# Optimization experiments

Measured on AMD Instinct MI355X. Metric: run time of the kernel, lower is better.

## Reference

```python
import jax, jax.numpy as jnp
import numpy as np

NEG_INF = -1000000000.0
B, N, D, H, L, DFF = 4, 1024, 512, 8, 6, 2048
DH = D // H
R2 = 10.0 ** 2  # locality_radius^2
EPS = 1e-5


def setup_inputs() -> dict:
    key = jax.random.key(0)
    ks = jax.random.split(key, 16)
    s = 0.02
    inp = {
        "tokens": jax.random.normal(ks[0], (B, N, D), jnp.float32),
        "xy": jax.random.uniform(ks[1], (B, N, 2), jnp.float32) * 100.0,
        "Wq": jax.random.normal(ks[2], (L, D, D), jnp.float32) * s,
        "Wk": jax.random.normal(ks[3], (L, D, D), jnp.float32) * s,
        "Wv": jax.random.normal(ks[4], (L, D, D), jnp.float32) * s,
        "Wo": jax.random.normal(ks[5], (L, D, D), jnp.float32) * s,
        "bo": jnp.zeros((L, D), jnp.float32),
        "W1": jax.random.normal(ks[6], (L, D, DFF), jnp.float32) * s,
        "b1": jnp.zeros((L, DFF), jnp.float32),
        "W2": jax.random.normal(ks[7], (L, DFF, D), jnp.float32) * s,
        "b2": jnp.zeros((L, D), jnp.float32),
        "g1": jnp.ones((L, D), jnp.float32),
        "be1": jnp.zeros((L, D), jnp.float32),
        "g2": jnp.ones((L, D), jnp.float32),
        "be2": jnp.zeros((L, D), jnp.float32),
        "gf": jnp.ones((D,), jnp.float32),
        "bf": jnp.zeros((D,), jnp.float32),
        "alive": jax.random.randint(ks[8], (B, N), 0, 2, dtype=jnp.int32),
        "species": jax.random.randint(ks[9], (B, N), 0, 3, dtype=jnp.int32),
        "n_agents": 512,
    }
    return inp


def _ln(x, g, b):
    m = jnp.mean(x, axis=-1, keepdims=True)
    v = jnp.mean((x - m) ** 2, axis=-1, keepdims=True)
    return (x - m) * jax.lax.rsqrt(v + EPS) * g + b


def _build_bias(alive, xy, species, dtype):
    # (B,1,N,N) additive bias, broadcast over heads (original repeats per head)
    af = alive.astype(dtype)
    bias = (1.0 - af)[:, None, None, :] * NEG_INF  # dead keys
    d2 = jnp.sum((xy[:, :, None, :] - xy[:, None, :, :]) ** 2, axis=-1)  # (B,N,N)
    bias = bias + jnp.where(d2 > R2, NEG_INF, 0.0)[:, None, :, :]
    ia = species < 2
    ip = species == 2
    ct = (ia[:, :, None] & ip[:, None, :]) | (ip[:, :, None] & ia[:, None, :])
    bias = bias + jnp.where(ct, NEG_INF, 0.0)[:, None, :, :]
    return bias


def reference(tokens, xy, Wq, Wk, Wv, Wo, bo, W1, b1, W2, b2,
              g1, be1, g2, be2, gf, bf, alive, species, n_agents):
    bias = _build_bias(alive, xy, species, tokens.dtype)
    scale = np.float32(np.sqrt(DH))
    x = tokens
    for l in range(L):
        h = _ln(x, g1[l], be1[l])
        q = (h @ Wq[l]).reshape(B, N, H, DH)
        k = (h @ Wk[l]).reshape(B, N, H, DH)
        v = (h @ Wv[l]).reshape(B, N, H, DH)
        scores = jnp.einsum('bihd,bjhd->bhij', q, k) / scale + bias
        w = jax.nn.softmax(scores, axis=-1)
        o = jnp.einsum('bhij,bjhd->bihd', w, v).reshape(B, N, D)
        x = x + (o @ Wo[l] + bo[l])
        h2 = _ln(x, g2[l], be2[l])
        ff = jax.nn.gelu(h2 @ W1[l] + b1[l], approximate=False) @ W2[l] + b2[l]
        x = x + ff
    return _ln(x, gf, bf)
```

## Files before the change

### kernel.cpp

```cpp
#include <hip/hip_runtime.h>
#include <math.h>

namespace {

constexpr int B = 4, N = 1024, D = 512, H = 8, DHd = 64, L = 6, DFFd = 2048;
constexpr int M = B * N;
constexpr int QKVS = 3 * D;
constexpr float NEG = -1000000000.0f;
constexpr float R2c = 100.0f;

typedef __attribute__((ext_vector_type(8))) short bf16x8;
typedef __attribute__((ext_vector_type(4))) float f32x4;

__device__ __forceinline__ short f2bf(float f) {
  union { float f; unsigned u; } c; c.f = f;
  unsigned r = (c.u + 0x7fffu + ((c.u >> 16) & 1u)) >> 16;
  return (short)r;
}

__device__ __forceinline__ float gelu_f(float x) {
  return 0.5f * x * (1.0f + erff(x * 0.70710678118654752f));
}

__global__ __launch_bounds__(256) void bias_kernel(
    const float* __restrict__ xy, const int* __restrict__ alive,
    const int* __restrict__ species, float* __restrict__ bias)
{
  int j = blockIdx.x * 256 + threadIdx.x;
  int i = blockIdx.y;
  int b = blockIdx.z;
  float xi = xy[((size_t)b * N + i) * 2 + 0];
  float yi = xy[((size_t)b * N + i) * 2 + 1];
  float xj = xy[((size_t)b * N + j) * 2 + 0];
  float yj = xy[((size_t)b * N + j) * 2 + 1];
  float dx = xi - xj, dy = yi - yj;
  float d2 = dx * dx + dy * dy;
  float bv = 0.0f;
  if (alive[b * N + j] == 0) bv += NEG;
  if (d2 > R2c) bv += NEG;
  int si = species[b * N + i], sj = species[b * N + j];
  bool ia = si < 2, ip = si == 2, ja = sj < 2, jp = sj == 2;
  if ((ia && jp) || (ip && ja)) bv += NEG;
  bias[((size_t)b * N + i) * N + j] = bv;
}

__global__ __launch_bounds__(256) void wprep_kernel(
    const float* __restrict__ src, short* __restrict__ dst,
    int K, int Nc, size_t srcLS, size_t dstLS)
{
  __shared__ float t[32][33];
  int k0 = blockIdx.x * 32, n0 = blockIdx.y * 32;
  src += (size_t)blockIdx.z * srcLS;
  dst += (size_t)blockIdx.z * dstLS;
  int r = threadIdx.x >> 5, c = threadIdx.x & 31;
#pragma unroll
  for (int i = 0; i < 4; ++i)
    t[r + i * 8][c] = src[(size_t)(k0 + r + i * 8) * Nc + n0 + c];
  __syncthreads();
#pragma unroll
  for (int i = 0; i < 4; ++i)
    dst[(size_t)(n0 + r + i * 8) * K + k0 + c] = f2bf(t[c][r + i * 8]);
}

__global__ __launch_bounds__(64) void ln_kernel(
    const float* __restrict__ x, const float* __restrict__ g,
    const float* __restrict__ be, float* __restrict__ outf,
    short* __restrict__ outb)
{
  int row = blockIdx.x;
  int tid = threadIdx.x;
  const float* xr = x + (size_t)row * D;
  float v[8];
  float sum = 0.f;
#pragma unroll
  for (int i = 0; i < 8; ++i) { v[i] = xr[tid + i * 64]; sum += v[i]; }
#pragma unroll
  for (int off = 32; off > 0; off >>= 1) sum += __shfl_down(sum, off);
  sum = __shfl(sum, 0);
  float mean = sum * (1.0f / D);
  float vs = 0.f;
#pragma unroll
  for (int i = 0; i < 8; ++i) { float d = v[i] - mean; vs += d * d; }
#pragma unroll
  for (int off = 32; off > 0; off >>= 1) vs += __shfl_down(vs, off);
  vs = __shfl(vs, 0);
  float rstd = rsqrtf(vs * (1.0f / D) + 1e-5f);
#pragma unroll
  for (int i = 0; i < 8; ++i) {
    int c = tid + i * 64;
    float o = (v[i] - mean) * rstd * g[c] + be[c];
    if (outb) outb[(size_t)row * D + c] = f2bf(o);
    else      outf[(size_t)row * D + c] = o;
  }
}

template <int BN, int NJ>
__global__ __launch_bounds__(256) void gemm_db_kernel(
    const short* __restrict__ A, const short* __restrict__ Bt,
    const float* __restrict__ bvec, float* __restrict__ Cf,
    short* __restrict__ Cb, int K, int Nc, int mode)
{
  __shared__ __align__(16) short As[2][128 * 32];
  __shared__ __align__(16) short Bs[2][BN * 32];
  const int bm = blockIdx.y * 128, bn = blockIdx.x * BN;
  const int t = threadIdx.x, wave = t >> 6, lane = t & 63;
  const int quad = lane >> 4, ln16 = lane & 15;
  const int wm = (wave & 1) * 64, wn = (wave >> 1) * (16 * NJ);
  const int srow = lane >> 2, sseg = lane & 3;
  constexpr int PEND = 2 + BN / 64;

  const short* Abase = A + (size_t)(bm + wave * 16 + srow) * K + sseg * 8;
  const short* Bbase = Bt + (size_t)(bn + wave * 16 + srow) * K + sseg * 8;
  const int nk = K >> 5;

  auto issue = [&](int p, int k0) {
#pragma unroll
    for (int h2 = 0; h2 < 2; ++h2) {
      __builtin_amdgcn_global_load_lds(
          (const __attribute__((address_space(1))) void*)(Abase + (size_t)h2 * 64 * K + k0),
          (__attribute__((address_space(3))) void*)&As[p][(wave * 16 + h2 * 64) * 32],
          16, 0, 0);
    }
#pragma unroll
    for (int h2 = 0; h2 < BN / 64; ++h2) {
      __builtin_amdgcn_global_load_lds(
          (const __attribute__((address_space(1))) void*)(Bbase + (size_t)h2 * 64 * K + k0),
          (__attribute__((address_space(3))) void*)&Bs[p][(wave * 16 + h2 * 64) * 32],
          16, 0, 0);
    }
  };

  f32x4 acc[4][NJ];
#pragma unroll
  for (int i = 0; i < 4; ++i)
#pragma unroll
    for (int j = 0; j < NJ; ++j) acc[i][j] = (f32x4){0.f, 0.f, 0.f, 0.f};

  issue(0, 0);
  for (int kt = 0; kt < nk; ++kt) {
    const int p = kt & 1;
    if (kt + 1 < nk) {
      issue(p ^ 1, (kt + 1) << 5);
      asm volatile("s_waitcnt vmcnt(%0)" :: "i"(PEND) : "memory");
    } else {
      asm volatile("s_waitcnt vmcnt(0)" ::: "memory");
    }
    asm volatile("s_barrier" ::: "memory");
    bf16x8 af[4], bfr[NJ];
#pragma unroll
    for (int i = 0; i < 4; ++i)
      af[i] = *(const bf16x8*)&As[p][(wm + i * 16 + ln16) * 32 + quad * 8];
#pragma unroll
    for (int j = 0; j < NJ; ++j)
      bfr[j] = *(const bf16x8*)&Bs[p][(wn + j * 16 + ln16) * 32 + quad * 8];
#pragma unroll
    for (int i = 0; i < 4; ++i)
#pragma unroll
      for (int j = 0; j < NJ; ++j)
        acc[i][j] = __builtin_amdgcn_mfma_f32_16x16x32_bf16(af[i], bfr[j], acc[i][j], 0, 0, 0);
    asm volatile("s_barrier" ::: "memory");
  }

  const int colbase = bn + wn + ln16;
#pragma unroll
  for (int i = 0; i < 4; ++i) {
#pragma unroll
    for (int r = 0; r < 4; ++r) {
      size_t row = (size_t)(bm + wm + i * 16 + quad * 4 + r);
      size_t off = row * Nc + colbase;
      if (mode == 0) {
#pragma unroll
        for (int j = 0; j < NJ; ++j) Cb[off + j * 16] = f2bf(acc[i][j][r]);
      } else if (mode == 1) {
#pragma unroll
        for (int j = 0; j < NJ; ++j) {
          float o = acc[i][j][r] + bvec[colbase + j * 16] + Cf[off + j * 16];
          Cf[off + j * 16] = o;
        }
      } else {
#pragma unroll
        for (int j = 0; j < NJ; ++j)
          Cb[off + j * 16] = f2bf(gelu_f(acc[i][j][r] + bvec[colbase + j * 16]));
      }
    }
  }
}

__global__ __launch_bounds__(256) void attn_mfma_kernel(
    const short* __restrict__ qkv, const float* __restrict__ bias,
    short* __restrict__ o)
{
  constexpr int LDR = 72;
  __shared__ __align__(16) short Qs[64 * LDR];
  __shared__ __align__(16) short Ks[2][64 * LDR];
  __shared__ __align__(16) short Vt[2][64 * LDR];
  __shared__ __align__(16) short Ps[4 * 16 * LDR];

  const int q0 = blockIdx.x * 64;
  const int hh = blockIdx.y;
  const int b  = blockIdx.z;
  const int t  = threadIdx.x;
  const int wave = t >> 6;
  const int lane = t & 63;
  const int quad = lane >> 4;
  const int ln16 = lane & 15;
  const int srow = t >> 2, sseg = t & 3;

  {
    const short* qb = qkv + (size_t)(b * N + q0 + srow) * QKVS + hh * 64 + sseg * 16;
    *(bf16x8*)&Qs[srow * LDR + sseg * 16] = *(const bf16x8*)qb;
    *(bf16x8*)&Qs[srow * LDR + sseg * 16 + 8] = *(const bf16x8*)(qb + 8);
  }
  __syncthreads();

  const int qrow = wave * 16 + ln16;
  const bf16x8 qf0 = *(const bf16x8*)&Qs[qrow * LDR + quad * 8];
  const bf16x8 qf1 = *(const bf16x8*)&Qs[qrow * LDR + 32 + quad * 8];

  float m_run = -1e30f, l_run = 0.f;
  f32x4 Oacc[4];
#pragma unroll
  for (int dt = 0; dt < 4; ++dt) Oacc[dt] = (f32x4){0.f, 0.f, 0.f, 0.f};

  short* Psw = Ps + wave * 16 * LDR;
  const float* brow = bias + (size_t)(b * N + q0 + wave * 16 + ln16) * N;
  const short* kb0 = qkv + (size_t)b * N * QKVS + 512 + hh * 64 + sseg * 16;
  const short* vb0 = qkv + (size_t)b * N * QKVS + 1024 + hh * 64 + sseg * 16;

  bf16x8 k0r = *(const bf16x8*)(kb0 + (size_t)srow * QKVS);
  bf16x8 k1r = *(const bf16x8*)(kb0 + (size_t)srow * QKVS + 8);
  bf16x8 v0r = *(const bf16x8*)(vb0 + (size_t)srow * QKVS);
  bf16x8 v1r = *(const bf16x8*)(vb0 + (size_t)srow * QKVS + 8);
  float4 b4[4];
#pragma unroll
  for (int ks = 0; ks < 4; ++ks)
    b4[ks] = *(const float4*)&brow[ks * 16 + quad * 4];

  for (int kt = 0; kt < 16; ++kt) {
    const int p = kt & 1;
    *(bf16x8*)&Ks[p][srow * LDR + sseg * 16] = k0r;
    *(bf16x8*)&Ks[p][srow * LDR + sseg * 16 + 8] = k1r;
#pragma unroll
    for (int e = 0; e < 8; ++e) {
      Vt[p][(sseg * 16 + e) * LDR + srow] = v0r[e];
      Vt[p][(sseg * 16 + 8 + e) * LDR + srow] = v1r[e];
    }
    const int k0n = (kt + 1 < 16) ? (kt + 1) * 64 : 0;
    bf16x8 nk0 = *(const bf16x8*)(kb0 + (size_t)(k0n + srow) * QKVS);
    bf16x8 nk1 = *(const bf16x8*)(kb0 + (size_t)(k0n + srow) * QKVS + 8);
    bf16x8 nv0 = *(const bf16x8*)(vb0 + (size_t)(k0n + srow) * QKVS);
    bf16x8 nv1 = *(const bf16x8*)(vb0 + (size_t)(k0n + srow) * QKVS + 8);
    float4 bcur[4] = {b4[0], b4[1], b4[2], b4[3]};
#pragma unroll
    for (int ks = 0; ks < 4; ++ks)
      b4[ks] = *(const float4*)&brow[k0n + ks * 16 + quad * 4];
    asm volatile("s_waitcnt lgkmcnt(0)\n\ts_barrier" ::: "memory");

    float sv[4][4];
#pragma unroll
    for (int ks = 0; ks < 4; ++ks) {
      bf16x8 a0 = *(const bf16x8*)&Ks[p][(ks * 16 + ln16) * LDR + quad * 8];
      bf16x8 a1 = *(const bf16x8*)&Ks[p][(ks * 16 + ln16) * LDR + 32 + quad * 8];
      f32x4 z = (f32x4){0.f, 0.f, 0.f, 0.f};
      z = __builtin_amdgcn_mfma_f32_16x16x32_bf16(a0, qf0, z, 0, 0, 0);
      z = __builtin_amdgcn_mfma_f32_16x16x32_bf16(a1, qf1, z, 0, 0, 0);
#pragma unroll
      for (int r = 0; r < 4; ++r)
        sv[ks][r] = z[r] * 0.125f + (&bcur[ks].x)[r];
    }

    float mt = sv[0][0];
#pragma unroll
    for (int ks = 0; ks < 4; ++ks)
#pragma unroll
      for (int r = 0; r < 4; ++r) mt = fmaxf(mt, sv[ks][r]);
    mt = fmaxf(mt, __shfl_xor(mt, 16));
    mt = fmaxf(mt, __shfl_xor(mt, 32));
    const float m_new = fmaxf(m_run, mt);
    const float alpha = __expf(m_run - m_new);
    m_run = m_new;
    float rs = 0.f;
    float pv[4][4];
#pragma unroll
    for (int ks = 0; ks < 4; ++ks)
#pragma unroll
      for (int r = 0; r < 4; ++r) {
        float e = __expf(sv[ks][r] - m_new);
        pv[ks][r] = e;
        rs += e;
      }
    rs += __shfl_xor(rs, 16);
    rs += __shfl_xor(rs, 32);
    l_run = l_run * alpha + rs;
    float af[4];
#pragma unroll
    for (int r = 0; r < 4; ++r) af[r] = __shfl(alpha, quad * 4 + r);
#pragma unroll
    for (int dt = 0; dt < 4; ++dt)
#pragma unroll
      for (int r = 0; r < 4; ++r) Oacc[dt][r] *= af[r];

#pragma unroll
    for (int ks = 0; ks < 4; ++ks) {
      short4 pk = {f2bf(pv[ks][0]), f2bf(pv[ks][1]), f2bf(pv[ks][2]), f2bf(pv[ks][3])};
      *(short4*)&Psw[ln16 * LDR + ks * 16 + quad * 4] = pk;
    }

    bf16x8 ap0 = *(const bf16x8*)&Psw[ln16 * LDR + quad * 8];
    bf16x8 ap1 = *(const bf16x8*)&Psw[ln16 * LDR + 32 + quad * 8];
#pragma unroll
    for (int dt = 0; dt < 4; ++dt) {
      bf16x8 bv0 = *(const bf16x8*)&Vt[p][(dt * 16 + ln16) * LDR + quad * 8];
      bf16x8 bv1 = *(const bf16x8*)&Vt[p][(dt * 16 + ln16) * LDR + 32 + quad * 8];
      Oacc[dt] = __builtin_amdgcn_mfma_f32_16x16x32_bf16(ap0, bv0, Oacc[dt], 0, 0, 0);
      Oacc[dt] = __builtin_amdgcn_mfma_f32_16x16x32_bf16(ap1, bv1, Oacc[dt], 0, 0, 0);
    }

    k0r = nk0; k1r = nk1; v0r = nv0; v1r = nv1;
  }

  const float linv = 1.0f / l_run;
  float iv[4];
#pragma unroll
  for (int r = 0; r < 4; ++r) iv[r] = __shfl(linv, quad * 4 + r);
#pragma unroll
  for (int dt = 0; dt < 4; ++dt) {
#pragma unroll
    for (int r = 0; r < 4; ++r) {
      int row = q0 + wave * 16 + quad * 4 + r;
      o[(size_t)(b * N + row) * D + hh * 64 + dt * 16 + ln16] =
          f2bf(Oacc[dt][r] * iv[r]);
    }
  }
}

}

extern "C" void kernel_launch(void* const* d_in, const int* in_sizes, int n_in,
                              void* d_out, int out_size, void* d_ws, size_t ws_size,
                              hipStream_t stream)
{
  const float* tokens  = (const float*)d_in[0];
  const float* xy      = (const float*)d_in[1];
  const float* Wq      = (const float*)d_in[2];
  const float* Wk      = (const float*)d_in[3];
  const float* Wv      = (const float*)d_in[4];
  const float* Wo      = (const float*)d_in[5];
  const float* bo      = (const float*)d_in[6];
  const float* W1      = (const float*)d_in[7];
  const float* b1      = (const float*)d_in[8];
  const float* W2      = (const float*)d_in[9];
  const float* b2      = (const float*)d_in[10];
  const float* g1      = (const float*)d_in[11];
  const float* be1     = (const float*)d_in[12];
  const float* g2      = (const float*)d_in[13];
  const float* be2     = (const float*)d_in[14];
  const float* gf      = (const float*)d_in[15];
  const float* bf      = (const float*)d_in[16];
  const int*   alive   = (const int*)d_in[17];
  const int*   species = (const int*)d_in[18];

  char* p = (char*)d_ws;
  float* bias = (float*)p; p += (size_t)B * N * N * 4;
  float* x    = (float*)p; p += (size_t)M * D * 4;
  short* h    = (short*)p; p += (size_t)M * D * 2;
  short* qkv  = (short*)p; p += (size_t)M * DFFd * 2;
  short* ff   = qkv;
  short* Wqkvt = (short*)p; p += (size_t)L * QKVS * D * 2;
  short* Wot   = (short*)p; p += (size_t)L * D * D * 2;
  short* W1t   = (short*)p; p += (size_t)L * DFFd * D * 2;
  short* W2t   = (short*)p; p += (size_t)L * D * DFFd * 2;

  hipMemcpyAsync(x, tokens, sizeof(float) * (size_t)M * D,
                 hipMemcpyDeviceToDevice, stream);
  bias_kernel<<<dim3(N / 256, N, B), 256, 0, stream>>>(xy, alive, species, bias);

  wprep_kernel<<<dim3(16, 16, L), 256, 0, stream>>>(
      Wq, Wqkvt + (size_t)0 * D * D, D, D, (size_t)D * D, (size_t)QKVS * D);
  wprep_kernel<<<dim3(16, 16, L), 256, 0, stream>>>(
      Wk, Wqkvt + (size_t)1 * D * D, D, D, (size_t)D * D, (size_t)QKVS * D);
  wprep_kernel<<<dim3(16, 16, L), 256, 0, stream>>>(
      Wv, Wqkvt + (size_t)2 * D * D, D, D, (size_t)D * D, (size_t)QKVS * D);
  wprep_kernel<<<dim3(16, 16, L), 256, 0, stream>>>(
      Wo, Wot, D, D, (size_t)D * D, (size_t)D * D);
  wprep_kernel<<<dim3(16, 64, L), 256, 0, stream>>>(
      W1, W1t, D, DFFd, (size_t)D * DFFd, (size_t)DFFd * D);
  wprep_kernel<<<dim3(64, 16, L), 256, 0, stream>>>(
      W2, W2t, DFFd, D, (size_t)DFFd * D, (size_t)D * DFFd);

  for (int l = 0; l < L; ++l) {
    ln_kernel<<<M, 64, 0, stream>>>(x, g1 + l * D, be1 + l * D, nullptr, h);
    gemm_db_kernel<128, 4><<<dim3(QKVS / 128, M / 128), 256, 0, stream>>>(
        h, Wqkvt + (size_t)l * QKVS * D, nullptr, nullptr, qkv, D, QKVS, 0);
    attn_mfma_kernel<<<dim3(N / 64, H, B), 256, 0, stream>>>(qkv, bias, h);
    gemm_db_kernel<64, 2><<<dim3(D / 64, M / 128), 256, 0, stream>>>(
        h, Wot + (size_t)l * D * D, bo + l * D, x, nullptr, D, D, 1);
    ln_kernel<<<M, 64, 0, stream>>>(x, g2 + l * D, be2 + l * D, nullptr, h);
    gemm_db_kernel<128, 4><<<dim3(DFFd / 128, M / 128), 256, 0, stream>>>(
        h, W1t + (size_t)l * DFFd * D, b1 + l * DFFd, nullptr, ff, D, DFFd, 2);
    gemm_db_kernel<64, 2><<<dim3(D / 64, M / 128), 256, 0, stream>>>(
        ff, W2t + (size_t)l * D * DFFd, b2 + l * D, x, nullptr, DFFd, D, 1);
  }
  ln_kernel<<<M, 64, 0, stream>>>(x, gf, bf, (float*)d_out, nullptr);
}
```

Before: 1.038 ms.

## Replace GEMM with intra-block split-K over waves using 32x32 MFMA and LDS reduction

Replaces the double-buffered 128xBN GEMM with a 64x64-tile kernel in which each of four waves handles a quarter of K in its own private LDS slot, so the main loop needs no block-wide barriers. It switches to 32x32x16 bf16 MFMA, reduces the four partial tiles through LDS, and writes the epilogue with vectorized float4/short4 stores. Smaller tiles give more blocks, which helps the narrow N=512 GEMMs fill the GPU. The costs are lower arithmetic intensity (more global traffic per FLOP), a 68KB LDS footprint that limits occupancy, and extra reduction work.

```diff
diff --git a/kernel.cpp b/kernel.cpp
--- a/kernel.cpp
+++ b/kernel.cpp
@@ -11,6 +11,7 @@
 
 typedef __attribute__((ext_vector_type(8))) short bf16x8;
 typedef __attribute__((ext_vector_type(4))) float f32x4;
+typedef __attribute__((ext_vector_type(16))) float f32x16;
 
 __device__ __forceinline__ short f2bf(float f) {
   union { float f; unsigned u; } c; c.f = f;
@@ -94,94 +95,112 @@
   }
 }
 
-template <int BN, int NJ>
-__global__ __launch_bounds__(256) void gemm_db_kernel(
+__global__ __launch_bounds__(256, 2) void gemm_sk_kernel(
     const short* __restrict__ A, const short* __restrict__ Bt,
     const float* __restrict__ bvec, float* __restrict__ Cf,
     short* __restrict__ Cb, int K, int Nc, int mode)
 {
-  __shared__ __align__(16) short As[2][128 * 32];
-  __shared__ __align__(16) short Bs[2][BN * 32];
-  const int bm = blockIdx.y * 128, bn = blockIdx.x * BN;
+  __shared__ __align__(16) char smem[4 * 17408];
+  const int bm = blockIdx.y * 64, bn = blockIdx.x * 64;
   const int t = threadIdx.x, wave = t >> 6, lane = t & 63;
-  const int quad = lane >> 4, ln16 = lane & 15;
-  const int wm = (wave & 1) * 64, wn = (wave >> 1) * (16 * NJ);
-  const int srow = lane >> 2, sseg = lane & 3;
-  constexpr int PEND = 2 + BN / 64;
-
-  const short* Abase = A + (size_t)(bm + wave * 16 + srow) * K + sseg * 8;
-  const short* Bbase = Bt + (size_t)(bn + wave * 16 + srow) * K + sseg * 8;
-  const int nk = K >> 5;
-
-  auto issue = [&](int p, int k0) {
-#pragma unroll
-    for (int h2 = 0; h2 < 2; ++h2) {
+  const int half = lane >> 5;
+  const int l32 = lane & 31;
+  const int srow4 = lane >> 2, sseg4 = lane & 3;
+
+  char* slot = smem + wave * 17408;
+  const int kw0 = wave * (K >> 2);
+  const int nch = K >> 7;
+
+  const short* Ab = A + (size_t)(bm + srow4) * K + kw0 + sseg4 * 8;
+  const short* Bb = Bt + (size_t)(bn + srow4) * K + kw0 + sseg4 * 8;
+
+  auto issue = [&](int p, int kc) {
+    char* ab = slot + p * 8192;
+    char* bb = slot + p * 8192 + 4096;
+#pragma unroll
+    for (int i = 0; i < 4; ++i) {
       __builtin_amdgcn_global_load_lds(
-          (const __attribute__((address_space(1))) void*)(Abase + (size_t)h2 * 64 * K + k0),
-          (__attribute__((address_space(3))) void*)&As[p][(wave * 16 + h2 * 64) * 32],
-          16, 0, 0);
-    }
-#pragma unroll
-    for (int h2 = 0; h2 < BN / 64; ++h2) {
+          (const __attribute__((address_space(1))) void*)(Ab + (size_t)i * 16 * K + kc),
+          (__attribute__((address_space(3))) void*)(ab + i * 1024), 16, 0, 0);
+    }
+#pragma unroll
+    for (int i = 0; i < 4; ++i) {
       __builtin_amdgcn_global_load_lds(
-          (const __attribute__((address_space(1))) void*)(Bbase + (size_t)h2 * 64 * K + k0),
-          (__attribute__((address_space(3))) void*)&Bs[p][(wave * 16 + h2 * 64) * 32],
-          16, 0, 0);
+          (const __attribute__((address_space(1))) void*)(Bb + (size_t)i * 16 * K + kc),
+          (__attribute__((address_space(3))) void*)(bb + i * 1024), 16, 0, 0);
     }
   };
 
-  f32x4 acc[4][NJ];
-#pragma unroll
-  for (int i = 0; i < 4; ++i)
-#pragma unroll
-    for (int j = 0; j < NJ; ++j) acc[i][j] = (f32x4){0.f, 0.f, 0.f, 0.f};
+  f32x16 acc[2][2];
+#pragma unroll
+  for (int i = 0; i < 2; ++i)
+#pragma unroll
+    for (int j = 0; j < 2; ++j)
+#pragma unroll
+      for (int r = 0; r < 16; ++r) acc[i][j][r] = 0.f;
 
   issue(0, 0);
-  for (int kt = 0; kt < nk; ++kt) {
-    const int p = kt & 1;
-    if (kt + 1 < nk) {
-      issue(p ^ 1, (kt + 1) << 5);
-      asm volatile("s_waitcnt vmcnt(%0)" :: "i"(PEND) : "memory");
+  for (int c = 0; c < nch; ++c) {
+    const int p = c & 1;
+    if (c + 1 < nch) {
+      issue(p ^ 1, (c + 1) * 32);
+      asm volatile("s_waitcnt vmcnt(%0)" :: "i"(8) : "memory");
     } else {
       asm volatile("s_waitcnt vmcnt(0)" ::: "memory");
     }
-    asm volatile("s_barrier" ::: "memory");
-    bf16x8 af[4], bfr[NJ];
-#pragma unroll
-    for (int i = 0; i < 4; ++i)
-      af[i] = *(const bf16x8*)&As[p][(wm + i * 16 + ln16) * 32 + quad * 8];
-#pragma unroll
-    for (int j = 0; j < NJ; ++j)
-      bfr[j] = *(const bf16x8*)&Bs[p][(wn + j * 16 + ln16) * 32 + quad * 8];
-#pragma unroll
-    for (int i = 0; i < 4; ++i)
-#pragma unroll
-      for (int j = 0; j < NJ; ++j)
-        acc[i][j] = __builtin_amdgcn_mfma_f32_16x16x32_bf16(af[i], bfr[j], acc[i][j], 0, 0, 0);
-    asm volatile("s_barrier" ::: "memory");
-  }
-
-  const int colbase = bn + wn + ln16;
-#pragma unroll
-  for (int i = 0; i < 4; ++i) {
-#pragma unroll
-    for (int r = 0; r < 4; ++r) {
-      size_t row = (size_t)(bm + wm + i * 16 + quad * 4 + r);
-      size_t off = row * Nc + colbase;
-      if (mode == 0) {
-#pragma unroll
-        for (int j = 0; j < NJ; ++j) Cb[off + j * 16] = f2bf(acc[i][j][r]);
-      } else if (mode == 1) {
-#pragma unroll
-        for (int j = 0; j < NJ; ++j) {
-          float o = acc[i][j][r] + bvec[colbase + j * 16] + Cf[off + j * 16];
-          Cf[off + j * 16] = o;
-        }
-      } else {
-#pragma unroll
-        for (int j = 0; j < NJ; ++j)
-          Cb[off + j * 16] = f2bf(gelu_f(acc[i][j][r] + bvec[colbase + j * 16]));
+    const short* As = (const short*)(slot + p * 8192);
+    const short* Bs = (const short*)(slot + p * 8192 + 4096);
+#pragma unroll
+    for (int ks = 0; ks < 2; ++ks) {
+      bf16x8 a0 = *(const bf16x8*)&As[(l32) * 32 + ks * 16 + half * 8];
+      bf16x8 a1 = *(const bf16x8*)&As[(32 + l32) * 32 + ks * 16 + half * 8];
+      bf16x8 b0 = *(const bf16x8*)&Bs[(l32) * 32 + ks * 16 + half * 8];
+      bf16x8 b1 = *(const bf16x8*)&Bs[(32 + l32) * 32 + ks * 16 + half * 8];
+      acc[0][0] = __builtin_amdgcn_mfma_f32_32x32x16_bf16(a0, b0, acc[0][0], 0, 0, 0);
+      acc[0][1] = __builtin_amdgcn_mfma_f32_32x32x16_bf16(a0, b1, acc[0][1], 0, 0, 0);
+      acc[1][0] = __builtin_amdgcn_mfma_f32_32x32x16_bf16(a1, b0, acc[1][0], 0, 0, 0);
+      acc[1][1] = __builtin_amdgcn_mfma_f32_32x32x16_bf16(a1, b1, acc[1][1], 0, 0, 0);
+    }
+  }
+
+  float* red = (float*)slot;
+#pragma unroll
+  for (int ti = 0; ti < 2; ++ti)
+#pragma unroll
+    for (int tj = 0; tj < 2; ++tj)
+#pragma unroll
+      for (int r = 0; r < 16; ++r) {
+        int row = ti * 32 + (r & 3) + 8 * (r >> 2) + 4 * half;
+        red[row * 68 + tj * 32 + l32] = acc[ti][tj][r];
       }
+  __syncthreads();
+
+  const int row = t >> 2, cs = (t & 3) * 16;
+  const size_t orow = (size_t)(bm + row) * Nc + bn + cs;
+#pragma unroll
+  for (int u = 0; u < 4; ++u) {
+    float4 s0 = *(const float4*)((const float*)(smem + 0 * 17408) + row * 68 + cs + u * 4);
+    float4 s1 = *(const float4*)((const float*)(smem + 1 * 17408) + row * 68 + cs + u * 4);
+    float4 s2 = *(const float4*)((const float*)(smem + 2 * 17408) + row * 68 + cs + u * 4);
+    float4 s3 = *(const float4*)((const float*)(smem + 3 * 17408) + row * 68 + cs + u * 4);
+    float o0 = s0.x + s1.x + s2.x + s3.x;
+    float o1 = s0.y + s1.y + s2.y + s3.y;
+    float o2 = s0.z + s1.z + s2.z + s3.z;
+    float o3 = s0.w + s1.w + s2.w + s3.w;
+    const int col = bn + cs + u * 4;
+    if (mode == 0) {
+      short4 w = {f2bf(o0), f2bf(o1), f2bf(o2), f2bf(o3)};
+      *(short4*)&Cb[orow + u * 4] = w;
+    } else if (mode == 1) {
+      float4 bv = *(const float4*)&bvec[col];
+      float4 rv = *(const float4*)&Cf[orow + u * 4];
+      float4 w = {o0 + bv.x + rv.x, o1 + bv.y + rv.y, o2 + bv.z + rv.z, o3 + bv.w + rv.w};
+      *(float4*)&Cf[orow + u * 4] = w;
+    } else {
+      float4 bv = *(const float4*)&bvec[col];
+      short4 w = {f2bf(gelu_f(o0 + bv.x)), f2bf(gelu_f(o1 + bv.y)),
+                  f2bf(gelu_f(o2 + bv.z)), f2bf(gelu_f(o3 + bv.w))};
+      *(short4*)&Cb[orow + u * 4] = w;
     }
   }
 }
@@ -390,15 +409,15 @@
 
   for (int l = 0; l < L; ++l) {
     ln_kernel<<<M, 64, 0, stream>>>(x, g1 + l * D, be1 + l * D, nullptr, h);
-    gemm_db_kernel<128, 4><<<dim3(QKVS / 128, M / 128), 256, 0, stream>>>(
+    gemm_sk_kernel<<<dim3(QKVS / 64, M / 64), 256, 0, stream>>>(
         h, Wqkvt + (size_t)l * QKVS * D, nullptr, nullptr, qkv, D, QKVS, 0);
     attn_mfma_kernel<<<dim3(N / 64, H, B), 256, 0, stream>>>(qkv, bias, h);
-    gemm_db_kernel<64, 2><<<dim3(D / 64, M / 128), 256, 0, stream>>>(
+    gemm_sk_kernel<<<dim3(D / 64, M / 64), 256, 0, stream>>>(
         h, Wot + (size_t)l * D * D, bo + l * D, x, nullptr, D, D, 1);
     ln_kernel<<<M, 64, 0, stream>>>(x, g2 + l * D, be2 + l * D, nullptr, h);
-    gemm_db_kernel<128, 4><<<dim3(DFFd / 128, M / 128), 256, 0, stream>>>(
+    gemm_sk_kernel<<<dim3(DFFd / 64, M / 64), 256, 0, stream>>>(
         h, W1t + (size_t)l * DFFd * D, b1 + l * DFFd, nullptr, ff, D, DFFd, 2);
-    gemm_db_kernel<64, 2><<<dim3(D / 64, M / 128), 256, 0, stream>>>(
+    gemm_sk_kernel<<<dim3(D / 64, M / 64), 256, 0, stream>>>(
         ff, W2t + (size_t)l * D * DFFd, b2 + l * D, x, nullptr, DFFd, D, 1);
   }
   ln_kernel<<<M, 64, 0, stream>>>(x, gf, bf, (float*)d_out, nullptr);
```

After: 994.4 us. -4.2%, faster.
